# Optimization experiments

Measured on AMD Instinct MI355X. Metric: run time of the kernel, lower is better.

The kernel has to match this reference:

```python
import jax, jax.numpy as jnp
import numpy as np
from jax.experimental.ode import odeint

MAX_SEQ_LEN = 32
DELTA_T = 0.05
B, D, H = 512, 1024, 4096
W_SCALE = 0.02  # keep dynamics well-conditioned for the adaptive solver


def setup_inputs() -> dict:
    key = jax.random.key(0)
    k0, k1, k2 = jax.random.split(key, 3)
    x = jax.random.normal(k0, (B, D), dtype=jnp.float32)
    W1 = jax.random.normal(k1, (D, H), dtype=jnp.float32) * W_SCALE
    b1 = jnp.zeros((H,), dtype=jnp.float32)
    W2 = jax.random.normal(k2, (H, D), dtype=jnp.float32) * W_SCALE
    b2 = jnp.zeros((D,), dtype=jnp.float32)
    return {"x": x, "W1": W1, "b1": b1, "W2": W2, "b2": b2}


def reference(x, W1, b1, W2, b2):
    # flow_func.apply({'params': params}, y, t): autonomous 2-layer tanh MLP flow
    def flow(y, t):
        return jnp.tanh(y @ W1 + b1) @ W2 + b2  # [B, D]

    time = jnp.arange(0, MAX_SEQ_LEN, dtype=jnp.float32) * DELTA_T  # [T]
    # dopri5 adaptive integration; output stacks the state at each time point
    final_states = odeint(flow, x, time)  # [T, B, D]
    return final_states
```

## Files before the change

### kernel.cpp

```cpp
#include <hip/hip_runtime.h>
#include <hip/hip_bf16.h>
#include <cstdint>
#include <cstddef>


#define GAS __attribute__((address_space(1)))
#define LAS __attribute__((address_space(3)))

typedef __bf16 bf16x8 __attribute__((ext_vector_type(8)));
typedef float  f32x4  __attribute__((ext_vector_type(4)));
typedef unsigned short u16;

struct P {
  const float *x, *W1, *b1, *W2, *b2;
  float* out;
  u16 *W1t, *W2t, *ybf, *ytbf, *Abuf;
  float *ya, *yb, *k1a, *k1b, *kb2, *kb3, *kb4;
};

__device__ __forceinline__ u16 f2bf(float f) {
  __hip_bfloat16 h = __float2bfloat16(f);
  return __builtin_bit_cast(u16, h);
}

__global__ __launch_bounds__(256) void transpose_bf16(
    const float* __restrict__ W, u16* __restrict__ Wt, int K, int N) {
  __shared__ u16 tile[32][33];
  int kb = blockIdx.x << 5, nb = blockIdx.y << 5;
  int tx = threadIdx.x & 31, ty = threadIdx.x >> 5;
  #pragma unroll
  for (int i = 0; i < 32; i += 8)
    tile[ty + i][tx] = f2bf(W[(size_t)(kb + ty + i) * N + nb + tx]);
  __syncthreads();
  #pragma unroll
  for (int i = 0; i < 32; i += 8)
    Wt[(size_t)(nb + ty + i) * K + kb + tx] = tile[tx][ty + i];
}

__global__ __launch_bounds__(256) void init_state(P p) {
  int i = blockIdx.x * 256 + threadIdx.x;
  float4 v = reinterpret_cast<const float4*>(p.x)[i];
  reinterpret_cast<float4*>(p.ya)[i] = v;
  reinterpret_cast<float4*>(p.out)[i] = v;
  reinterpret_cast<ushort4*>(p.ybf)[i] =
      make_ushort4(f2bf(v.x), f2bf(v.y), f2bf(v.z), f2bf(v.w));
}

__device__ __forceinline__ void stage64(
    const u16* __restrict__ A, const u16* __restrict__ Bt,
    char* AsB, char* BsB, int kt, int ldk, int tid) {
  #pragma unroll
  for (int i = 0; i < 2; ++i) {
    int j = i * 256 + tid;
    int row = j >> 3, slot = j & 7, kc = slot ^ (row & 7);
    __builtin_amdgcn_global_load_lds(
        (const GAS void*)(A + (size_t)row * ldk + kt + kc * 8),
        (LAS void*)(AsB + j * 16), 16, 0, 0);
  }
  #pragma unroll
  for (int i = 0; i < 2; ++i) {
    int j = i * 256 + tid;
    int row = j >> 3, slot = j & 7, kc = slot ^ (row & 7);
    __builtin_amdgcn_global_load_lds(
        (const GAS void*)(Bt + (size_t)row * ldk + kt + kc * 8),
        (LAS void*)(BsB + j * 16), 16, 0, 0);
  }
}

__device__ __forceinline__ bf16x8 frag64(const char* base, int row, int g) {
  return *(const bf16x8*)(base + row * 128 + ((g ^ (row & 7)) << 4));
}

__device__ __forceinline__ void stage32w(
    const u16* __restrict__ src, int ldk, char* dst, int lane) {
  #pragma unroll
  for (int c = 0; c < 2; ++c) {
    int j = c * 64 + lane;
    int row = j >> 2, slot = j & 3;
    int kc = slot ^ ((row >> 1) & 3);
    __builtin_amdgcn_global_load_lds(
        (const GAS void*)(src + (size_t)row * ldk + kc * 8),
        (LAS void*)(dst + j * 16), 16, 0, 0);
  }
}

__device__ __forceinline__ bf16x8 frag32(const char* base, int row, int g) {
  return *(const bf16x8*)(base + row * 64 + ((g ^ ((row >> 1) & 3)) << 4));
}

__global__ __launch_bounds__(256) void g1_k(P p, const u16* __restrict__ st) {
  __shared__ __attribute__((aligned(16))) char L[2][16384];
  const int tid = threadIdx.x, lane = tid & 63, wid = tid >> 6;
  const int mh = wid >> 1, nh = wid & 1;
  const int b = blockIdx.x, xcd = b & 7, r = b >> 3;
  const int nt = xcd * 8 + (r & 7), mt = r >> 3;
  const int m0 = mt * 64, n0 = nt * 64;
  const int lrow = lane & 15, kgrp = lane >> 4;

  f32x4 acc[2][2];
  #pragma unroll
  for (int mi = 0; mi < 2; ++mi)
    #pragma unroll
    for (int ni = 0; ni < 2; ++ni) acc[mi][ni] = (f32x4){0.f, 0.f, 0.f, 0.f};

  const u16* Asrc = st + (size_t)m0 * 1024;
  const u16* Bsrc = p.W1t + (size_t)n0 * 1024;
  stage64(Asrc, Bsrc, L[0], L[0] + 8192, 0, 1024, tid);
  __syncthreads();
  int cur = 0;
  for (int t = 0; t < 16; ++t) {
    if (t + 1 < 16)
      stage64(Asrc, Bsrc, L[cur ^ 1], L[cur ^ 1] + 8192, (t + 1) * 64, 1024, tid);
    const char* As = L[cur];
    const char* Bs = L[cur] + 8192;
    #pragma unroll
    for (int ks = 0; ks < 2; ++ks) {
      bf16x8 af[2], bf[2];
      #pragma unroll
      for (int mi = 0; mi < 2; ++mi)
        af[mi] = frag64(As, mh * 32 + mi * 16 + lrow, ks * 4 + kgrp);
      #pragma unroll
      for (int ni = 0; ni < 2; ++ni)
        bf[ni] = frag64(Bs, nh * 32 + ni * 16 + lrow, ks * 4 + kgrp);
      #pragma unroll
      for (int mi = 0; mi < 2; ++mi)
        #pragma unroll
        for (int ni = 0; ni < 2; ++ni)
          acc[mi][ni] = __builtin_amdgcn_mfma_f32_16x16x32_bf16(
              af[mi], bf[ni], acc[mi][ni], 0, 0, 0);
    }
    __syncthreads();
    cur ^= 1;
  }

  #pragma unroll
  for (int mi = 0; mi < 2; ++mi)
    #pragma unroll
    for (int ni = 0; ni < 2; ++ni) {
      int gcol = n0 + nh * 32 + ni * 16 + lrow;
      float bb = p.b1[gcol];
      #pragma unroll
      for (int r_ = 0; r_ < 4; ++r_) {
        int grow = m0 + mh * 32 + mi * 16 + kgrp * 4 + r_;
        p.Abuf[(size_t)grow * 4096 + gcol] = f2bf(tanhf(acc[mi][ni][r_] + bb));
      }
    }
}

__global__ __launch_bounds__(512, 1) void g2c_k(P p, int n, int e) {
  __shared__ __attribute__((aligned(16))) char L[98304];
  const int tid = threadIdx.x, lane = tid & 63, w = tid >> 6;
  const int kq = w >> 1, nh = w & 1;
  const int b = blockIdx.x, xcd = b & 7, r = b >> 3;
  const int ntile = xcd * 2 + (r & 1), mt = r >> 1;
  const int m0 = mt * 32;
  const int nbase = ntile * 64 + nh * 32;
  const int lrow = lane & 15, kgrp = lane >> 4;
  const int MN = 524288;
  char* wbase = L + w * 12288;

  f32x4 acc[2][2];
  #pragma unroll
  for (int mi = 0; mi < 2; ++mi)
    #pragma unroll
    for (int ni = 0; ni < 2; ++ni) acc[mi][ni] = (f32x4){0.f, 0.f, 0.f, 0.f};

  const u16* Asrc = p.Abuf + (size_t)m0 * 4096 + kq * 1024;
  const u16* Bsrc = p.W2t + (size_t)nbase * 4096 + kq * 1024;

#define STG(t)                                                      \
  {                                                                 \
    char* rb = wbase + ((t) % 3) * 4096;                            \
    stage32w(Asrc + (t) * 32, 4096, rb, lane);                      \
    stage32w(Bsrc + (t) * 32, 4096, rb + 2048, lane);               \
  }

  STG(0);
  STG(1);
  for (int t = 0; t < 32; ++t) {
    if (t + 2 < 32) {
      STG(t + 2);
      asm volatile("s_waitcnt vmcnt(8)" ::: "memory");
    } else if (t + 1 < 32) {
      asm volatile("s_waitcnt vmcnt(4)" ::: "memory");
    } else {
      asm volatile("s_waitcnt vmcnt(0)" ::: "memory");
    }
    __builtin_amdgcn_sched_barrier(0);
    const char* rb = wbase + (t % 3) * 4096;
    bf16x8 af[2], bf[2];
    af[0] = frag32(rb, lrow, kgrp);
    af[1] = frag32(rb, 16 + lrow, kgrp);
    bf[0] = frag32(rb + 2048, lrow, kgrp);
    bf[1] = frag32(rb + 2048, 16 + lrow, kgrp);
    #pragma unroll
    for (int mi = 0; mi < 2; ++mi)
      #pragma unroll
      for (int ni = 0; ni < 2; ++ni)
        acc[mi][ni] = __builtin_amdgcn_mfma_f32_16x16x32_bf16(
            af[mi], bf[ni], acc[mi][ni], 0, 0, 0);
  }
#undef STG

  __syncthreads();
  float* sc = (float*)L;
  if (kq > 0) {
    #pragma unroll
    for (int mi = 0; mi < 2; ++mi)
      #pragma unroll
      for (int ni = 0; ni < 2; ++ni)
        #pragma unroll
        for (int r_ = 0; r_ < 4; ++r_)
          sc[((kq - 1) * 2 + nh) * 1024 + (mi * 16 + kgrp * 4 + r_) * 32 +
             ni * 16 + lrow] = acc[mi][ni][r_];
  }
  __syncthreads();
  if (kq != 0) return;

  #pragma unroll
  for (int mi = 0; mi < 2; ++mi)
    #pragma unroll
    for (int ni = 0; ni < 2; ++ni)
      #pragma unroll
      for (int r_ = 0; r_ < 4; ++r_) {
        int idx = (mi * 16 + kgrp * 4 + r_) * 32 + ni * 16 + lrow;
        #pragma unroll
        for (int pw = 0; pw < 3; ++pw)
          acc[mi][ni][r_] += sc[(pw * 2 + nh) * 1024 + idx];
      }

  const float h = 0.775f;
  const float h6 = h / 6.f;
  const float coef = (e == 3) ? h : h * 0.5f;
  const float* yin = (n & 1) ? p.yb : p.ya;
  float* yout = (n & 1) ? p.ya : p.yb;
  const float* y0p = (n & 1) ? p.ya : p.yb;
  float* k1buf = (n & 1) ? p.k1b : p.k1a;
  const float* k1prev = (n & 1) ? p.k1a : p.k1b;
  float* kbuf = (e == 1) ? k1buf : (e == 2 ? p.kb2 : p.kb3);

  #pragma unroll
  for (int mi = 0; mi < 2; ++mi) {
    #pragma unroll
    for (int ni = 0; ni < 2; ++ni) {
      const int gcol = nbase + ni * 16 + lrow;
      const float bb = p.b2[gcol];
      #pragma unroll
      for (int r_ = 0; r_ < 4; ++r_) {
        int grow = m0 + mi * 16 + kgrp * 4 + r_;
        size_t gi = (size_t)grow * 1024 + gcol;
        float F = acc[mi][ni][r_] + bb;
        float yv = yin[gi];
        if (e < 4) {
          kbuf[gi] = F;
          float nv = yv + coef * F;
          p.ytbf[gi] = f2bf(nv);
          if (e == 1 && n >= 1) {
            float yA = y0p[gi];
            float yB = yv;
            float f0 = k1prev[gi];
            #pragma unroll
            for (int j = 1; j <= 15; ++j) {
              float th = 0.05f * j / h;
              float t2 = th * th, t3 = t2 * th;
              float c0 = 2.f * t3 - 3.f * t2 + 1.f;
              float c1 = (t3 - 2.f * t2 + th) * h;
              float c2 = 3.f * t2 - 2.f * t3;
              float c3 = (t3 - t2) * h;
              p.out[(size_t)j * MN + gi] =
                  c0 * yA + c1 * f0 + c2 * yB + c3 * F;
            }
          }
        } else {
          if (n == 1) p.kb4[gi] = F;
          float nv = yv + h6 * (k1buf[gi] + 2.f * p.kb2[gi] +
                                2.f * p.kb3[gi] + F);
          yout[gi] = nv;
          if (n == 1) p.out[(size_t)31 * MN + gi] = nv;
          p.ybf[gi] = f2bf(nv);
        }
      }
    }
  }
}

__global__ __launch_bounds__(256) void tail_k(P p) {
  const int MN = 524288;
  const float h = 0.775f;
  int i = blockIdx.x * 256 + threadIdx.x;
  float yA = p.yb[i];
  float yB = p.ya[i];
  float f0 = p.k1b[i];
  float f1 = p.kb4[i];
  #pragma unroll
  for (int j = 16; j < 31; ++j) {
    float th = (0.05f * j - h) / h;
    float t2 = th * th, t3 = t2 * th;
    float c0 = 2.f * t3 - 3.f * t2 + 1.f;
    float c1 = (t3 - 2.f * t2 + th) * h;
    float c2 = 3.f * t2 - 2.f * t3;
    float c3 = (t3 - t2) * h;
    p.out[(size_t)j * MN + i] = c0 * yA + c1 * f0 + c2 * yB + c3 * f1;
  }
}

extern "C" void kernel_launch(void* const* d_in, const int* in_sizes, int n_in,
                              void* d_out, int out_size, void* d_ws, size_t ws_size,
                              hipStream_t stream) {
  P p;
  p.x  = (const float*)d_in[0];
  p.W1 = (const float*)d_in[1];
  p.b1 = (const float*)d_in[2];
  p.W2 = (const float*)d_in[3];
  p.b2 = (const float*)d_in[4];
  p.out = (float*)d_out;

  const int Dq = 1024, Hq = 4096;
  const int MN = 512 * 1024;
  char* ws = (char*)d_ws;
  size_t off = 0;
  p.W1t  = (u16*)(ws + off);   off += (size_t)Hq * Dq * 2;
  p.W2t  = (u16*)(ws + off);   off += (size_t)Dq * Hq * 2;
  p.ya   = (float*)(ws + off); off += (size_t)MN * 4;
  p.yb   = (float*)(ws + off); off += (size_t)MN * 4;
  p.ybf  = (u16*)(ws + off);   off += (size_t)MN * 2;
  p.ytbf = (u16*)(ws + off);   off += (size_t)MN * 2;
  p.Abuf = (u16*)(ws + off);   off += (size_t)512 * Hq * 2;
  p.k1a  = (float*)(ws + off); off += (size_t)MN * 4;
  p.k1b  = (float*)(ws + off); off += (size_t)MN * 4;
  p.kb2  = (float*)(ws + off); off += (size_t)MN * 4;
  p.kb3  = (float*)(ws + off); off += (size_t)MN * 4;
  p.kb4  = (float*)(ws + off); off += (size_t)MN * 4;
  if (ws_size < off) return;

  transpose_bf16<<<dim3(Dq / 32, Hq / 32), 256, 0, stream>>>(p.W1, p.W1t, Dq, Hq);
  transpose_bf16<<<dim3(Hq / 32, Dq / 32), 256, 0, stream>>>(p.W2, p.W2t, Hq, Dq);
  init_state<<<MN / 4 / 256, 256, 0, stream>>>(p);

  for (int n = 0; n < 2; ++n) {
    for (int e = 1; e <= 4; ++e) {
      g1_k<<<512, 256, 0, stream>>>(p, (e == 1) ? p.ybf : p.ytbf);
      g2c_k<<<256, 512, 0, stream>>>(p, n, e);
    }
  }
  tail_k<<<MN / 256, 256, 0, stream>>>(p);
}
```

Baseline: 302.8 us.

## Merge setup kernels, fuse tail interpolation into last RK stage, vectorize epilogue

Combines the two weight transposes and the state init into one launch, and moves the second-step Hermite interpolation from a separate tail kernel into the final g2c stage, which removes the kb4 buffer. The split-K reduction now has all four K-quarter waves write partials to LDS, and every thread reduces and finishes one float4 of outputs. Before, one quarter of the waves handled the epilogue with scalar accesses. This trims launch overhead and extra global traffic, and uses all waves in the epilogue, at the cost of an extra LDS partial write.

```diff
diff --git a/kernel.cpp b/kernel.cpp
--- a/kernel.cpp
+++ b/kernel.cpp
@@ -15,7 +15,7 @@
   const float *x, *W1, *b1, *W2, *b2;
   float* out;
   u16 *W1t, *W2t, *ybf, *ytbf, *Abuf;
-  float *ya, *yb, *k1a, *k1b, *kb2, *kb3, *kb4;
+  float *ya, *yb, *k1a, *k1b, *kb2, *kb3;
 };
 
 __device__ __forceinline__ u16 f2bf(float f) {
@@ -23,27 +23,36 @@
   return __builtin_bit_cast(u16, h);
 }
 
-__global__ __launch_bounds__(256) void transpose_bf16(
-    const float* __restrict__ W, u16* __restrict__ Wt, int K, int N) {
-  __shared__ u16 tile[32][33];
-  int kb = blockIdx.x << 5, nb = blockIdx.y << 5;
-  int tx = threadIdx.x & 31, ty = threadIdx.x >> 5;
+__device__ __forceinline__ void tr_tile(
+    const float* __restrict__ W, u16* __restrict__ Wt, int K, int N,
+    int t, int tid, u16* s ) {
+  const int ntk = K >> 5;
+  const int kb = (t % ntk) << 5, nb = (t / ntk) << 5;
+  const int tx = tid & 31, ty = tid >> 5;
   #pragma unroll
   for (int i = 0; i < 32; i += 8)
-    tile[ty + i][tx] = f2bf(W[(size_t)(kb + ty + i) * N + nb + tx]);
+    s[(ty + i) * 33 + tx] = f2bf(W[(size_t)(kb + ty + i) * N + nb + tx]);
   __syncthreads();
   #pragma unroll
   for (int i = 0; i < 32; i += 8)
-    Wt[(size_t)(nb + ty + i) * K + kb + tx] = tile[tx][ty + i];
-}
-
-__global__ __launch_bounds__(256) void init_state(P p) {
-  int i = blockIdx.x * 256 + threadIdx.x;
-  float4 v = reinterpret_cast<const float4*>(p.x)[i];
-  reinterpret_cast<float4*>(p.ya)[i] = v;
-  reinterpret_cast<float4*>(p.out)[i] = v;
-  reinterpret_cast<ushort4*>(p.ybf)[i] =
-      make_ushort4(f2bf(v.x), f2bf(v.y), f2bf(v.z), f2bf(v.w));
+    Wt[(size_t)(nb + ty + i) * K + kb + tx] = s[tx * 33 + ty + i];
+}
+
+__global__ __launch_bounds__(256) void setup_k(P p) {
+  __shared__ u16 s[32 * 33];
+  const int b = blockIdx.x, tid = threadIdx.x;
+  if (b < 4096) {
+    tr_tile(p.W1, p.W1t, 1024, 4096, b, tid, s);
+  } else if (b < 8192) {
+    tr_tile(p.W2, p.W2t, 4096, 1024, b - 4096, tid, s);
+  } else {
+    int i = (b - 8192) * 256 + tid;
+    float4 v = reinterpret_cast<const float4*>(p.x)[i];
+    reinterpret_cast<float4*>(p.ya)[i] = v;
+    reinterpret_cast<float4*>(p.out)[i] = v;
+    reinterpret_cast<ushort4*>(p.ybf)[i] =
+        make_ushort4(f2bf(v.x), f2bf(v.y), f2bf(v.z), f2bf(v.w));
+  }
 }
 
 __device__ __forceinline__ void stage64(
@@ -156,7 +165,7 @@
   const int m0 = mt * 32;
   const int nbase = ntile * 64 + nh * 32;
   const int lrow = lane & 15, kgrp = lane >> 4;
-  const int MN = 524288;
+  const int q4 = 131072;
   char* wbase = L + w * 12288;
 
   f32x4 acc[2][2];
@@ -204,30 +213,27 @@
 
   __syncthreads();
   float* sc = (float*)L;
-  if (kq > 0) {
-    #pragma unroll
-    for (int mi = 0; mi < 2; ++mi)
-      #pragma unroll
-      for (int ni = 0; ni < 2; ++ni)
-        #pragma unroll
-        for (int r_ = 0; r_ < 4; ++r_)
-          sc[((kq - 1) * 2 + nh) * 1024 + (mi * 16 + kgrp * 4 + r_) * 32 +
-             ni * 16 + lrow] = acc[mi][ni][r_];
-  }
+  #pragma unroll
+  for (int mi = 0; mi < 2; ++mi)
+    #pragma unroll
+    for (int ni = 0; ni < 2; ++ni)
+      #pragma unroll
+      for (int r_ = 0; r_ < 4; ++r_)
+        sc[(kq * 2 + nh) * 1024 + (mi * 16 + kgrp * 4 + r_) * 32 +
+           ni * 16 + lrow] = acc[mi][ni][r_];
   __syncthreads();
-  if (kq != 0) return;
-
-  #pragma unroll
-  for (int mi = 0; mi < 2; ++mi)
-    #pragma unroll
-    for (int ni = 0; ni < 2; ++ni)
-      #pragma unroll
-      for (int r_ = 0; r_ < 4; ++r_) {
-        int idx = (mi * 16 + kgrp * 4 + r_) * 32 + ni * 16 + lrow;
-        #pragma unroll
-        for (int pw = 0; pw < 3; ++pw)
-          acc[mi][ni][r_] += sc[(pw * 2 + nh) * 1024 + idx];
-      }
+
+  const int t4 = tid * 4;
+  const int row = t4 >> 6, col = t4 & 63;
+  const int nh2 = col >> 5, cc = col & 31;
+  f32x4 s = (f32x4){0.f, 0.f, 0.f, 0.f};
+  #pragma unroll
+  for (int q_ = 0; q_ < 4; ++q_)
+    s += *(const f32x4*)(sc + (q_ * 2 + nh2) * 1024 + row * 32 + cc);
+
+  const int grow = m0 + row;
+  const int gcol = ntile * 64 + col;
+  const size_t gi4 = ((size_t)grow * 1024 + gcol) >> 2;
 
   const float h = 0.775f;
   const float h6 = h / 6.f;
@@ -239,68 +245,66 @@
   const float* k1prev = (n & 1) ? p.k1a : p.k1b;
   float* kbuf = (e == 1) ? k1buf : (e == 2 ? p.kb2 : p.kb3);
 
-  #pragma unroll
-  for (int mi = 0; mi < 2; ++mi) {
-    #pragma unroll
-    for (int ni = 0; ni < 2; ++ni) {
-      const int gcol = nbase + ni * 16 + lrow;
-      const float bb = p.b2[gcol];
-      #pragma unroll
-      for (int r_ = 0; r_ < 4; ++r_) {
-        int grow = m0 + mi * 16 + kgrp * 4 + r_;
-        size_t gi = (size_t)grow * 1024 + gcol;
-        float F = acc[mi][ni][r_] + bb;
-        float yv = yin[gi];
-        if (e < 4) {
-          kbuf[gi] = F;
-          float nv = yv + coef * F;
-          p.ytbf[gi] = f2bf(nv);
-          if (e == 1 && n >= 1) {
-            float yA = y0p[gi];
-            float yB = yv;
-            float f0 = k1prev[gi];
-            #pragma unroll
-            for (int j = 1; j <= 15; ++j) {
-              float th = 0.05f * j / h;
-              float t2 = th * th, t3 = t2 * th;
-              float c0 = 2.f * t3 - 3.f * t2 + 1.f;
-              float c1 = (t3 - 2.f * t2 + th) * h;
-              float c2 = 3.f * t2 - 2.f * t3;
-              float c3 = (t3 - t2) * h;
-              p.out[(size_t)j * MN + gi] =
-                  c0 * yA + c1 * f0 + c2 * yB + c3 * F;
-            }
-          }
-        } else {
-          if (n == 1) p.kb4[gi] = F;
-          float nv = yv + h6 * (k1buf[gi] + 2.f * p.kb2[gi] +
-                                2.f * p.kb3[gi] + F);
-          yout[gi] = nv;
-          if (n == 1) p.out[(size_t)31 * MN + gi] = nv;
-          p.ybf[gi] = f2bf(nv);
-        }
+  float4 bb = ((const float4*)p.b2)[gcol >> 2];
+  float4 F = make_float4(s[0] + bb.x, s[1] + bb.y, s[2] + bb.z, s[3] + bb.w);
+  float4 yv = ((const float4*)yin)[gi4];
+  float4* o4 = (float4*)p.out;
+
+  if (e < 4) {
+    ((float4*)kbuf)[gi4] = F;
+    float4 nv = make_float4(yv.x + coef * F.x, yv.y + coef * F.y,
+                            yv.z + coef * F.z, yv.w + coef * F.w);
+    ((ushort4*)p.ytbf)[gi4] =
+        make_ushort4(f2bf(nv.x), f2bf(nv.y), f2bf(nv.z), f2bf(nv.w));
+    if (e == 1 && n == 1) {
+      float4 yA = ((const float4*)y0p)[gi4];
+      float4 f0 = ((const float4*)k1prev)[gi4];
+      #pragma unroll
+      for (int j = 1; j <= 15; ++j) {
+        float th = 0.05f * j / h;
+        float t2 = th * th, t3 = t2 * th;
+        float c0 = 2.f * t3 - 3.f * t2 + 1.f;
+        float c1 = (t3 - 2.f * t2 + th) * h;
+        float c2 = 3.f * t2 - 2.f * t3;
+        float c3 = (t3 - t2) * h;
+        float4 o;
+        o.x = c0 * yA.x + c1 * f0.x + c2 * yv.x + c3 * F.x;
+        o.y = c0 * yA.y + c1 * f0.y + c2 * yv.y + c3 * F.y;
+        o.z = c0 * yA.z + c1 * f0.z + c2 * yv.z + c3 * F.z;
+        o.w = c0 * yA.w + c1 * f0.w + c2 * yv.w + c3 * F.w;
+        o4[(size_t)j * q4 + gi4] = o;
       }
     }
-  }
-}
-
-__global__ __launch_bounds__(256) void tail_k(P p) {
-  const int MN = 524288;
-  const float h = 0.775f;
-  int i = blockIdx.x * 256 + threadIdx.x;
-  float yA = p.yb[i];
-  float yB = p.ya[i];
-  float f0 = p.k1b[i];
-  float f1 = p.kb4[i];
-  #pragma unroll
-  for (int j = 16; j < 31; ++j) {
-    float th = (0.05f * j - h) / h;
-    float t2 = th * th, t3 = t2 * th;
-    float c0 = 2.f * t3 - 3.f * t2 + 1.f;
-    float c1 = (t3 - 2.f * t2 + th) * h;
-    float c2 = 3.f * t2 - 2.f * t3;
-    float c3 = (t3 - t2) * h;
-    p.out[(size_t)j * MN + i] = c0 * yA + c1 * f0 + c2 * yB + c3 * f1;
+  } else {
+    float4 a = ((const float4*)k1buf)[gi4];
+    float4 c = ((const float4*)p.kb2)[gi4];
+    float4 d = ((const float4*)p.kb3)[gi4];
+    float4 nv;
+    nv.x = yv.x + h6 * (a.x + 2.f * c.x + 2.f * d.x + F.x);
+    nv.y = yv.y + h6 * (a.y + 2.f * c.y + 2.f * d.y + F.y);
+    nv.z = yv.z + h6 * (a.z + 2.f * c.z + 2.f * d.z + F.z);
+    nv.w = yv.w + h6 * (a.w + 2.f * c.w + 2.f * d.w + F.w);
+    ((float4*)yout)[gi4] = nv;
+    ((ushort4*)p.ybf)[gi4] =
+        make_ushort4(f2bf(nv.x), f2bf(nv.y), f2bf(nv.z), f2bf(nv.w));
+    if (n == 1) {
+      o4[(size_t)31 * q4 + gi4] = nv;
+      #pragma unroll
+      for (int j = 16; j <= 30; ++j) {
+        float th = (0.05f * j - h) / h;
+        float t2 = th * th, t3 = t2 * th;
+        float c0 = 2.f * t3 - 3.f * t2 + 1.f;
+        float c1 = (t3 - 2.f * t2 + th) * h;
+        float c2 = 3.f * t2 - 2.f * t3;
+        float c3 = (t3 - t2) * h;
+        float4 o;
+        o.x = c0 * yv.x + c1 * a.x + c2 * nv.x + c3 * F.x;
+        o.y = c0 * yv.y + c1 * a.y + c2 * nv.y + c3 * F.y;
+        o.z = c0 * yv.z + c1 * a.z + c2 * nv.z + c3 * F.z;
+        o.w = c0 * yv.w + c1 * a.w + c2 * nv.w + c3 * F.w;
+        o4[(size_t)j * q4 + gi4] = o;
+      }
+    }
   }
 }
 
@@ -330,12 +334,9 @@
   p.k1b  = (float*)(ws + off); off += (size_t)MN * 4;
   p.kb2  = (float*)(ws + off); off += (size_t)MN * 4;
   p.kb3  = (float*)(ws + off); off += (size_t)MN * 4;
-  p.kb4  = (float*)(ws + off); off += (size_t)MN * 4;
   if (ws_size < off) return;
 
-  transpose_bf16<<<dim3(Dq / 32, Hq / 32), 256, 0, stream>>>(p.W1, p.W1t, Dq, Hq);
-  transpose_bf16<<<dim3(Hq / 32, Dq / 32), 256, 0, stream>>>(p.W2, p.W2t, Hq, Dq);
-  init_state<<<MN / 4 / 256, 256, 0, stream>>>(p);
+  setup_k<<<8704, 256, 0, stream>>>(p);
 
   for (int n = 0; n < 2; ++n) {
     for (int e = 1; e <= 4; ++e) {
@@ -343,5 +344,4 @@
       g2c_k<<<256, 512, 0, stream>>>(p, n, e);
     }
   }
-  tail_k<<<MN / 256, 256, 0, stream>>>(p);
-}
+}
```

Result: faster. 261.3 us (-13.7%).
